# Kernel tuning notes

Measured on AMD Instinct MI355X. Metric: run time of the kernel, lower is better.

Reference implementation:

```python
import jax, jax.numpy as jnp
import numpy as np
from jax.scipy.special import logsumexp

L, B, C, H = 1024, 256, 96, 768
STD = (1.0 / C) ** 0.5


def setup_inputs() -> dict:
    key = jax.random.key(0)
    ks = jax.random.split(key, 8)
    emit = jax.random.normal(ks[0], (L, B, C), dtype=jnp.float32)
    hidden = jax.random.normal(ks[1], (B, H), dtype=jnp.float32)
    target = jax.random.randint(ks[2], (L, B), 0, C)
    # variable sentence lengths in [L//2, L]; mask[0] is always True
    lens = jax.random.randint(ks[3], (B,), L // 2, L + 1)
    mask = jnp.arange(L)[:, None] < lens[None, :]
    Wt = jax.random.normal(ks[4], (C * C, H), dtype=jnp.float32) * STD
    bt = jnp.zeros((C * C,), dtype=jnp.float32)
    Ws = jax.random.normal(ks[5], (C, H), dtype=jnp.float32) * STD
    bs = jnp.zeros((C,), dtype=jnp.float32)
    We = jax.random.normal(ks[6], (C, H), dtype=jnp.float32) * STD
    be = jnp.zeros((C,), dtype=jnp.float32)
    return {"emit": emit, "hidden": hidden, "target": target, "mask": mask,
            "Wt": Wt, "bt": bt, "Ws": Ws, "bs": bs, "We": We, "be": be}


def _crf_loss(emit, hidden, target, mask, Wt, bt, Ws, bs, We, be):
    l, b, c = emit.shape
    trans = (hidden @ Wt.T + bt).reshape(b, c, c)          # [B, prev, next]
    t_start = hidden @ Ws.T + bs                           # [B, C]
    t_end = hidden @ We.T + be                             # [B, C]

    # ---- log partition (forward algorithm), sequential scan over time ----
    def step(log_alpha, xs):
        emit_i, mask_i = xs                                # [B,C], [B]
        # scores[b,p,n] = log_alpha[b,p] + trans[b,p,n] + emit_i[b,n]
        new = logsumexp(log_alpha[:, :, None] + trans + emit_i[:, None, :], axis=1)
        log_alpha = jnp.where(mask_i[:, None], new, log_alpha)
        return log_alpha, None

    log_alpha0 = emit[0] + t_start
    log_alpha, _ = jax.lax.scan(step, log_alpha0, (emit[1:], mask[1:]))
    log_z = logsumexp(log_alpha + t_end, axis=1).sum()

    # ---- gold path score ----
    bidx = jnp.arange(b)
    tr_sc = trans[bidx[None, :], target[:-1], target[1:]]          # [L-1, B]
    emit_sc = jnp.take_along_axis(emit, target[:, :, None], axis=2)[:, :, 0]  # [L, B]
    scores = emit_sc.at[1:].add(tr_sc)
    score = jnp.sum(scores * mask.astype(emit.dtype))
    ends = mask.sum(axis=0) - 1                                    # [B]
    last_tag = target[ends, bidx]
    score = score + t_start[bidx, target[0]].sum() + t_end[bidx, last_tag].sum()

    return (log_z - score) / b


def reference(emit, hidden, target, mask, Wt, bt, Ws, bs, We, be):
    return _crf_loss(emit, hidden, target, mask, Wt, bt, Ws, bs, We, be)
```

## Files before the change

### kernel.cpp

```cpp
#include <hip/hip_runtime.h>
#include <hip/hip_bf16.h>
#include <stdint.h>

#define LL 1024
#define BB 256
#define CC 96
#define HH 768
#define NW 9216
#define NTOT 9408
#define SEGS 8
#define SEGLEN 128
#define CHPB 15

typedef __attribute__((ext_vector_type(4))) float floatx4;
typedef __attribute__((ext_vector_type(2))) float floatx2;
typedef __attribute__((ext_vector_type(8))) short short8;

#define KAPPA 0x1p-16f
#define NEG_LOG_KAPPA 11.090354888959125f

__device__ __forceinline__ unsigned short f2bf(float f) {
  uint32_t u = __float_as_uint(f);
  return (unsigned short)((u + 0x7FFFu + ((u >> 16) & 1u)) >> 16);
}

#define GA_LD 40

__global__ __launch_bounds__(256) void gemm_mfma(
    const float* __restrict__ hidden, const float* __restrict__ Wt,
    const float* __restrict__ Ws, const float* __restrict__ We,
    const float* __restrict__ bt, const float* __restrict__ bs,
    const float* __restrict__ be, float* __restrict__ trans,
    float* __restrict__ tstart, float* __restrict__ tend) {
  __shared__ __align__(16) unsigned short As[128 * GA_LD];
  __shared__ __align__(16) unsigned short Bs[128 * GA_LD];
  const int t = threadIdx.x;
  const int lane = t & 63, wid = t >> 6;
  const int wm = wid >> 1, wn = wid & 1;
  const int l15 = lane & 15, qd = lane >> 4;
  const int m0 = blockIdx.y * 128, n0 = blockIdx.x * 128;
  const int srow = t >> 1, shalf = t & 1;

  floatx4 acc[4][4];
#pragma unroll
  for (int i = 0; i < 4; ++i)
#pragma unroll
    for (int j = 0; j < 4; ++j) acc[i][j] = (floatx4){0.f, 0.f, 0.f, 0.f};

  const int r = n0 + srow;
  const float* bsrc = (r < NW)        ? Wt + (size_t)r * HH
                      : (r < NW + CC) ? Ws + (size_t)(r - NW) * HH
                      : (r < NTOT)    ? We + (size_t)(r - NW - CC) * HH
                                      : nullptr;
  const float* asrc = hidden + (size_t)(m0 + srow) * HH;
  const int sidx = srow * GA_LD + shalf * 16;

  for (int k0 = 0; k0 < HH; k0 += 32) {
    __syncthreads();
    {
      const float4* s4 = (const float4*)(asrc + k0 + shalf * 16);
      uint32_t w[8];
#pragma unroll
      for (int u = 0; u < 4; ++u) {
        float4 v = s4[u];
        w[2 * u] = (uint32_t)f2bf(v.x) | ((uint32_t)f2bf(v.y) << 16);
        w[2 * u + 1] = (uint32_t)f2bf(v.z) | ((uint32_t)f2bf(v.w) << 16);
      }
      *(uint4*)&As[sidx] = make_uint4(w[0], w[1], w[2], w[3]);
      *(uint4*)&As[sidx + 8] = make_uint4(w[4], w[5], w[6], w[7]);
    }
    {
      uint32_t w[8];
      if (bsrc) {
        const float4* s4 = (const float4*)(bsrc + k0 + shalf * 16);
#pragma unroll
        for (int u = 0; u < 4; ++u) {
          float4 v = s4[u];
          w[2 * u] = (uint32_t)f2bf(v.x) | ((uint32_t)f2bf(v.y) << 16);
          w[2 * u + 1] = (uint32_t)f2bf(v.z) | ((uint32_t)f2bf(v.w) << 16);
        }
      } else {
#pragma unroll
        for (int u = 0; u < 8; ++u) w[u] = 0u;
      }
      *(uint4*)&Bs[sidx] = make_uint4(w[0], w[1], w[2], w[3]);
      *(uint4*)&Bs[sidx + 8] = make_uint4(w[4], w[5], w[6], w[7]);
    }
    __syncthreads();
    short8 af[4], bf[4];
#pragma unroll
    for (int i = 0; i < 4; ++i)
      af[i] = *(const short8*)&As[(64 * wm + 16 * i + l15) * GA_LD + qd * 8];
#pragma unroll
    for (int j = 0; j < 4; ++j)
      bf[j] = *(const short8*)&Bs[(64 * wn + 16 * j + l15) * GA_LD + qd * 8];
#pragma unroll
    for (int i = 0; i < 4; ++i)
#pragma unroll
      for (int j = 0; j < 4; ++j)
        acc[i][j] = __builtin_amdgcn_mfma_f32_16x16x32_bf16(af[i], bf[j],
                                                            acc[i][j], 0, 0, 0);
  }

#pragma unroll
  for (int j = 0; j < 4; ++j) {
    int n = n0 + 64 * wn + 16 * j + l15;
    if (n >= NTOT) continue;
    float bv;
    float* dst;
    int ldo;
    if (n < NW) {
      bv = bt[n]; dst = trans + n; ldo = NW;
    } else if (n < NW + CC) {
      bv = bs[n - NW]; dst = tstart + (n - NW); ldo = CC;
    } else {
      bv = be[n - NW - CC]; dst = tend + (n - NW - CC); ldo = CC;
    }
#pragma unroll
    for (int i = 0; i < 4; ++i)
#pragma unroll
      for (int rr = 0; rr < 4; ++rr) {
        int m = m0 + 64 * wm + 16 * i + 4 * qd + rr;
        dst[(size_t)m * ldo] = acc[i][j][rr] + bv;
      }
  }
}

__device__ __forceinline__ float wredf(float v) {
#pragma unroll
  for (int m = 32; m >= 1; m >>= 1) v += __shfl_xor(v, m);
  return v;
}
__device__ __forceinline__ int wredi(int v) {
#pragma unroll
  for (int m = 32; m >= 1; m >>= 1) v += __shfl_xor(v, m);
  return v;
}
__device__ __forceinline__ float bcast0(float x) {
  return __uint_as_float(__builtin_amdgcn_readfirstlane(__float_as_uint(x)));
}
__device__ __forceinline__ int get_len(const void* mask, int b, int l) {
  int cnt = 0;
  unsigned w0 = *(const unsigned*)mask;
  if (w0 == 1u) {
    const int* m32 = (const int*)mask;
    for (int i = l; i < LL; i += 64) cnt += (m32[i * BB + b] != 0);
  } else if (w0 == 0x01010101u) {
    const unsigned char* m8 = (const unsigned char*)mask;
    for (int i = l; i < LL; i += 64) cnt += (m8[i * BB + b] != 0);
  } else {
    const float* mf = (const float*)mask;
    for (int i = l; i < LL; i += 64) cnt += (mf[i * BB + b] != 0.f);
  }
  return wredi(cnt);
}

__global__ __launch_bounds__(64, 1) void crf_chain(
    const float* __restrict__ emit, const void* __restrict__ mask,
    const float* __restrict__ trans, const float* __restrict__ tstart,
    float* __restrict__ xvec, float* __restrict__ lsc) {
  const int blk = blockIdx.x;
  const int b = blk >> 3;
  const int k = blk & 7;
  const bool isfw = (k < 4);
  int segA, segB;
  bool hasB;
  if (isfw) {
    segA = k; segB = k + 4; hasB = true;
  } else if (k < 7) {
    segA = k - 3; segB = k + 1; hasB = true;
  } else {
    segA = 4; segB = 0; hasB = false;
  }
  const int l = threadIdx.x;
  const int pr = l >> 1, s = l & 1;

  __shared__ __align__(16) float ebA[2][8][CC];
  __shared__ __align__(16) float uAv[CC];
  __shared__ __align__(16) float ebB[2][8][CC];
  __shared__ __align__(16) float uBv[CC];

  const int len = get_len(mask, b, l);
  const int loA = segA * SEGLEN + 1;
  const int hiA = min((segA + 1) * SEGLEN, len - 1);
  const int loB = segB * SEGLEN + 1;
  const int hiB = hasB ? min((segB + 1) * SEGLEN, len - 1) : -1;
  const int cidA = b * CHPB + (isfw ? segA : 7 + segA);
  const int cidB = b * CHPB + (isfw ? segB : 7 + segB);
  const bool actB = hasB && (hiB >= loB);
  const int nA = hiA - loA + 1;
  const int nB = actB ? (hiB - loB + 1) : 0;

  if (hasB && !actB) {
    float* xo = xvec + (size_t)cidB * CC;
    xo[l] = 1.f;
    if (l < 32) xo[l + 64] = 1.f;
    if (l == 0) lsc[cidB] = 0.f;
  }
  if (hiA < loA) {
    float* xo = xvec + (size_t)cidA * CC;
    xo[l] = 1.f;
    if (l < 32) xo[l + 64] = 1.f;
    if (l == 0) lsc[cidA] = 0.f;
    return;
  }

  const float* tb = trans + (size_t)b * (CC * CC);
  floatx2 T2[3][24];
  if (isfw) {
#pragma unroll
    for (int j = 0; j < 24; ++j) {
      const float* r0 = tb + (48 * s + 2 * j) * CC + 3 * pr;
      const float* r1 = r0 + CC;
#pragma unroll
      for (int o = 0; o < 3; ++o)
        T2[o][j] = (floatx2){__expf(r0[o]), __expf(r1[o])};
    }
  } else {
#pragma unroll
    for (int o = 0; o < 3; ++o) {
      const float* row = tb + (3 * pr + o) * CC + 48 * s;
#pragma unroll
      for (int j = 0; j < 24; ++j)
        T2[o][j] = (floatx2){__expf(row[2 * j]), __expf(row[2 * j + 1])};
    }
  }

  const float4* e4 = (const float4*)emit;
  const int eoff = 3 * pr + 2 * s;
  float LA = 0.f, pvA = 1.f, LB = 0.f, pvB = 1.f;

#define CLOB asm volatile("" ::: "memory")

  auto STAGE = [&](float (*eb)[8][CC], int baserow, int slot) {
#pragma unroll
    for (int uu = 0; uu < 3; ++uu) {
      int v = l + 64 * uu;
      int rw = v / 24, c4 = v - 24 * rw;
      float4 vv = e4[((baserow + rw) * BB + b) * 24 + c4];
      floatx4 o = {__expf(vv.x) * KAPPA, __expf(vv.y) * KAPPA,
                   __expf(vv.z) * KAPPA, __expf(vv.w) * KAPPA};
      *(floatx4*)&eb[slot][rw][c4 * 4] = o;
    }
  };

  auto DOT = [&](const float* ub, float& a0, float& a1, float& a2) {
    const floatx4* up = (const floatx4*)&ub[48 * s];
    floatx2 A0 = {0.f, 0.f}, B0 = {0.f, 0.f};
    floatx2 A1 = {0.f, 0.f}, B1 = {0.f, 0.f};
    floatx2 A2 = {0.f, 0.f}, B2 = {0.f, 0.f};
#pragma unroll
    for (int j4 = 0; j4 < 12; ++j4) {
      floatx4 U = up[j4];
      floatx2 lo2 = {U.x, U.y}, hi2 = {U.z, U.w};
      A0 += lo2 * T2[0][2 * j4]; B0 += hi2 * T2[0][2 * j4 + 1];
      A1 += lo2 * T2[1][2 * j4]; B1 += hi2 * T2[1][2 * j4 + 1];
      A2 += lo2 * T2[2][2 * j4]; B2 += hi2 * T2[2][2 * j4 + 1];
    }
    floatx2 S0 = A0 + B0, S1 = A1 + B1, S2 = A2 + B2;
    a0 = S0.x + S0.y; a1 = S1.x + S1.y; a2 = S2.x + S2.y;
    a0 += __shfl_xor(a0, 1);
    a1 += __shfl_xor(a1, 1);
    a2 += __shfl_xor(a2, 1);
  };

  auto STEPF = [&](int i, int jjv, float& pvv, float& Lv,
                   float (*eb)[8][CC], float* ub) {
    float invP = 1.f;
    if ((jjv & 3) == 0) { invP = 1.0f / pvv; Lv += __logf(pvv); }
    float a0, a1, a2;
    DOT(ub, a0, a1, a2);
    floatx2 E = *(const floatx2*)&eb[(i >> 3) & 1][i & 7][eoff];
    float o0 = a0 * E.x * invP;
    if (((jjv + 1) & 3) == 0) pvv = bcast0(o0);
    if (s == 0) {
      floatx2 wv = {o0, a1 * E.y * invP};
      *(floatx2*)&ub[3 * pr] = wv;
    } else {
      ub[3 * pr + 2] = a2 * E.x * invP;
    }
  };

  auto STEPB = [&](int i, int lo, int jjv, float& pvv, float& Lv,
                   float (*eb)[8][CC], float* ub) {
    float invP = 1.f;
    if ((jjv & 3) == 0) { invP = 1.0f / pvv; Lv += __logf(pvv); }
    float a0, a1, a2;
    DOT(ub, a0, a1, a2);
    floatx2 E = (i > lo)
        ? *(const floatx2*)&eb[((i - 1) >> 3) & 1][(i - 1) & 7][eoff]
        : (floatx2){1.f, 1.f};
    float o0 = a0 * E.x * invP;
    if (((jjv + 1) & 3) == 0) pvv = bcast0(o0);
    if (s == 0) {
      floatx2 wv = {o0, a1 * E.y * invP};
      *(floatx2*)&ub[3 * pr] = wv;
    } else {
      ub[3 * pr + 2] = a2 * E.x * invP;
    }
  };

  if (isfw) {
    const int bA0 = loA & ~7;
    STAGE(ebA, bA0, (bA0 >> 3) & 1);
    if (actB) {
      const int bB0 = loB & ~7;
      STAGE(ebB, bB0, (bB0 >> 3) & 1);
    }
    if (segA == 0) {
      float a00 = emit[(size_t)b * CC] + tstart[b * CC];
      LA = a00;
      float v = emit[(size_t)b * CC + l] + tstart[b * CC + l];
      uAv[l] = __expf(v - a00);
      if (l < 32) {
        int c2 = l + 64;
        float v2 = emit[(size_t)b * CC + c2] + tstart[b * CC + c2];
        uAv[c2] = __expf(v2 - a00);
      }
    } else {
      uAv[l] = 1.f;
      if (l < 32) uAv[l + 64] = 1.f;
    }
    if (actB) {
      uBv[l] = 1.f;
      if (l < 32) uBv[l + 64] = 1.f;
    }
    CLOB;
    int jj = 1;
    int iA = loA, iB = loB;
    const int nmin = actB ? min(nA, nB) : 0;
    for (; jj <= nmin; ++jj, ++iA, ++iB) {
      bool st = false;
      if ((iA & 7) == 0) { STAGE(ebA, iA, (iA >> 3) & 1); st = true; }
      if ((iB & 7) == 0) { STAGE(ebB, iB, (iB >> 3) & 1); st = true; }
      if (st) CLOB;
      STEPF(iA, jj, pvA, LA, ebA, uAv);
      STEPF(iB, jj, pvB, LB, ebB, uBv);
      CLOB;
    }
    int jjA = jj;
    for (; iA <= hiA; ++iA, ++jjA) {
      if ((iA & 7) == 0) { STAGE(ebA, iA, (iA >> 3) & 1); CLOB; }
      STEPF(iA, jjA, pvA, LA, ebA, uAv);
      CLOB;
    }
    int jjB = jj;
    for (; actB && iB <= hiB; ++iB, ++jjB) {
      if ((iB & 7) == 0) { STAGE(ebB, iB, (iB >> 3) & 1); CLOB; }
      STEPF(iB, jjB, pvB, LB, ebB, uBv);
      CLOB;
    }
  } else {
    const int cA0 = hiA & ~7;
    STAGE(ebA, cA0, (cA0 >> 3) & 1);
    if (actB) {
      const int cB0 = hiB & ~7;
      STAGE(ebB, cB0, (cB0 >> 3) & 1);
    }
    CLOB;
    uAv[l] = ebA[(hiA >> 3) & 1][hiA & 7][l];
    if (l < 32) uAv[l + 64] = ebA[(hiA >> 3) & 1][hiA & 7][l + 64];
    if (actB) {
      uBv[l] = ebB[(hiB >> 3) & 1][hiB & 7][l];
      if (l < 32) uBv[l + 64] = ebB[(hiB >> 3) & 1][hiB & 7][l + 64];
    }
    CLOB;
    int jj = 1;
    int iA = hiA, iB = hiB;
    const int nmin = actB ? min(nA, nB) : 0;
    for (; jj <= nmin; ++jj, --iA, --iB) {
      bool st = false;
      if ((iA & 7) == 0 && iA > loA) {
        STAGE(ebA, iA - 8, ((iA >> 3) & 1) ^ 1); st = true;
      }
      if ((iB & 7) == 0 && iB > loB) {
        STAGE(ebB, iB - 8, ((iB >> 3) & 1) ^ 1); st = true;
      }
      if (st) CLOB;
      STEPB(iA, loA, jj, pvA, LA, ebA, uAv);
      STEPB(iB, loB, jj, pvB, LB, ebB, uBv);
      CLOB;
    }
    int jjA = jj;
    for (; iA >= loA; --iA, ++jjA) {
      if ((iA & 7) == 0 && iA > loA) {
        STAGE(ebA, iA - 8, ((iA >> 3) & 1) ^ 1); CLOB;
      }
      STEPB(iA, loA, jjA, pvA, LA, ebA, uAv);
      CLOB;
    }
    int jjB = jj;
    for (; actB && iB >= loB; --iB, ++jjB) {
      if ((iB & 7) == 0 && iB > loB) {
        STAGE(ebB, iB - 8, ((iB >> 3) & 1) ^ 1); CLOB;
      }
      STEPB(iB, loB, jjB, pvB, LB, ebB, uBv);
      CLOB;
    }
  }

  CLOB;
  {
    float* xo = xvec + (size_t)cidA * CC;
    xo[l] = uAv[l];
    if (l < 32) xo[l + 64] = uAv[l + 64];
    if (l == 0) lsc[cidA] = LA + (float)nA * NEG_LOG_KAPPA;
  }
  if (actB) {
    float* xo = xvec + (size_t)cidB * CC;
    xo[l] = uBv[l];
    if (l < 32) xo[l + 64] = uBv[l + 64];
    if (l == 0) lsc[cidB] = LB + (float)nB * NEG_LOG_KAPPA;
  }
}

__global__ __launch_bounds__(64) void crf_compose(
    const float* __restrict__ emit, const int* __restrict__ target,
    const void* __restrict__ mask, const float* __restrict__ trans,
    const float* __restrict__ tstart, const float* __restrict__ tend,
    const float* __restrict__ xvec, const float* __restrict__ lsc,
    float* __restrict__ out) {
  const int b = blockIdx.x;
  const int l = threadIdx.x;
  const int len = get_len(mask, b, l);

  float Lam = lsc[b * CHPB + 0];
  const float* xcur = xvec + (size_t)(b * CHPB + 0) * CC;
  for (int s2 = 1; s2 < SEGS; ++s2) {
    if (s2 * SEGLEN + 1 > len - 1) break;
    const float* bh = xvec + (size_t)(b * CHPB + (SEGS - 1) + s2) * CC;
    const float* ah = xvec + (size_t)(b * CHPB + s2) * CC;
    float pn = bh[l] * xcur[l];
    float pd = bh[l];
    if (l < 32) {
      pn += bh[l + 64] * xcur[l + 64];
      pd += bh[l + 64];
    }
    float num = wredf(pn), den = wredf(pd);
    Lam += __logf(num / den) + lsc[b * CHPB + s2];
    xcur = ah;
  }
  float zp = xcur[l] * __expf(tend[b * CC + l]);
  if (l < 32) zp += xcur[l + 64] * __expf(tend[b * CC + l + 64]);
  float logz = Lam + __logf(wredf(zp));

  const float* tb = trans + (size_t)b * (CC * CC);
  float sc = 0.f;
  for (int i = l; i < len; i += 64) {
    int tg = target[i * BB + b];
    sc += emit[((size_t)i * BB + b) * CC + tg];
    if (i >= 1) sc += tb[target[(i - 1) * BB + b] * CC + tg];
  }
  float score = wredf(sc);
  if (l == 0) {
    score += tstart[b * CC + target[b]] +
             tend[b * CC + target[(len - 1) * BB + b]];
    atomicAdd(out, (logz - score) * (1.0f / 256.0f));
  }
}

extern "C" void kernel_launch(void* const* d_in, const int* in_sizes, int n_in,
                              void* d_out, int out_size, void* d_ws, size_t ws_size,
                              hipStream_t stream) {
  const float* emit = (const float*)d_in[0];
  const float* hidden = (const float*)d_in[1];
  const int* target = (const int*)d_in[2];
  const void* mask = d_in[3];
  const float* Wt = (const float*)d_in[4];
  const float* bt = (const float*)d_in[5];
  const float* Ws = (const float*)d_in[6];
  const float* bs = (const float*)d_in[7];
  const float* We = (const float*)d_in[8];
  const float* be = (const float*)d_in[9];

  float* trans_ws = (float*)d_ws;
  float* ts_ws = trans_ws + (size_t)BB * CC * CC;
  float* te_ws = ts_ws + (size_t)BB * CC;
  float* xvec = te_ws + (size_t)BB * CC;
  float* lsc = xvec + (size_t)BB * CHPB * CC;

  hipMemsetAsync(d_out, 0, sizeof(float), stream);

  gemm_mfma<<<dim3((NTOT + 127) / 128, 2), 256, 0, stream>>>(
      hidden, Wt, Ws, We, bt, bs, be, trans_ws, ts_ws, te_ws);

  crf_chain<<<BB * 8, 64, 0, stream>>>(emit, mask, trans_ws, ts_ws, xvec, lsc);

  crf_compose<<<BB, 64, 0, stream>>>(emit, target, mask, trans_ws, ts_ws, te_ws,
                                     xvec, lsc, (float*)d_out);
}
```

Measured before the change: 442.3 us.

## Split chain dot across four lanes with DPP reduction and fused dual-chain step

```diff
diff --git a/kernel.cpp b/kernel.cpp
--- a/kernel.cpp
+++ b/kernel.cpp
@@ -139,6 +139,11 @@
 __device__ __forceinline__ float bcast0(float x) {
   return __uint_as_float(__builtin_amdgcn_readfirstlane(__float_as_uint(x)));
 }
+__device__ __forceinline__ float qsum4(float x) {
+  x += __int_as_float(__builtin_amdgcn_mov_dpp(__float_as_int(x), 0xB1, 0xF, 0xF, false));
+  x += __int_as_float(__builtin_amdgcn_mov_dpp(__float_as_int(x), 0x4E, 0xF, 0xF, false));
+  return x;
+}
 __device__ __forceinline__ int get_len(const void* mask, int b, int l) {
   int cnt = 0;
   unsigned w0 = *(const unsigned*)mask;
@@ -163,33 +168,28 @@
   const int b = blk >> 3;
   const int k = blk & 7;
   const bool isfw = (k < 4);
-  int segA, segB;
+  int segA, segB = 0;
   bool hasB;
-  if (isfw) {
-    segA = k; segB = k + 4; hasB = true;
-  } else if (k < 7) {
-    segA = k - 3; segB = k + 1; hasB = true;
-  } else {
-    segA = 4; segB = 0; hasB = false;
-  }
+  if (isfw) { segA = 2 * k; segB = 2 * k + 1; hasB = true; }
+  else if (k < 7) { segA = 2 * (k - 4) + 1; segB = segA + 1; hasB = true; }
+  else { segA = 7; hasB = false; }
   const int l = threadIdx.x;
-  const int pr = l >> 1, s = l & 1;
+  const int g = l >> 2, q = l & 3;
 
   __shared__ __align__(16) float ebA[2][8][CC];
-  __shared__ __align__(16) float uAv[CC];
+  __shared__ __align__(16) float uA[CC];
   __shared__ __align__(16) float ebB[2][8][CC];
-  __shared__ __align__(16) float uBv[CC];
+  __shared__ __align__(16) float uB[CC];
 
   const int len = get_len(mask, b, l);
   const int loA = segA * SEGLEN + 1;
   const int hiA = min((segA + 1) * SEGLEN, len - 1);
-  const int loB = segB * SEGLEN + 1;
+  const int loB = hasB ? segB * SEGLEN + 1 : 0;
   const int hiB = hasB ? min((segB + 1) * SEGLEN, len - 1) : -1;
+  const bool actA = hiA >= loA;
+  const bool actB = hasB && (hiB >= loB);
   const int cidA = b * CHPB + (isfw ? segA : 7 + segA);
-  const int cidB = b * CHPB + (isfw ? segB : 7 + segB);
-  const bool actB = hasB && (hiB >= loB);
-  const int nA = hiA - loA + 1;
-  const int nB = actB ? (hiB - loB + 1) : 0;
+  const int cidB = hasB ? (b * CHPB + (isfw ? segB : 7 + segB)) : 0;
 
   if (hasB && !actB) {
     float* xo = xvec + (size_t)cidB * CC;
@@ -197,204 +197,231 @@
     if (l < 32) xo[l + 64] = 1.f;
     if (l == 0) lsc[cidB] = 0.f;
   }
-  if (hiA < loA) {
+  if (!actA) {
     float* xo = xvec + (size_t)cidA * CC;
     xo[l] = 1.f;
     if (l < 32) xo[l + 64] = 1.f;
     if (l == 0) lsc[cidA] = 0.f;
     return;
   }
+  const int nA = hiA - loA + 1;
+  const int nB = actB ? (hiB - loB + 1) : 0;
 
   const float* tb = trans + (size_t)b * (CC * CC);
-  floatx2 T2[3][24];
+  floatx2 T2[6][12];
   if (isfw) {
 #pragma unroll
-    for (int j = 0; j < 24; ++j) {
-      const float* r0 = tb + (48 * s + 2 * j) * CC + 3 * pr;
-      const float* r1 = r0 + CC;
-#pragma unroll
-      for (int o = 0; o < 3; ++o)
-        T2[o][j] = (floatx2){__expf(r0[o]), __expf(r1[o])};
-    }
+    for (int t = 0; t < 6; ++t)
+#pragma unroll
+      for (int m = 0; m < 12; ++m) {
+        const float* p0 = tb + (24 * q + 2 * m) * CC + 6 * g + t;
+        T2[t][m] = (floatx2){__expf(p0[0]), __expf(p0[CC])};
+      }
   } else {
 #pragma unroll
-    for (int o = 0; o < 3; ++o) {
-      const float* row = tb + (3 * pr + o) * CC + 48 * s;
-#pragma unroll
-      for (int j = 0; j < 24; ++j)
-        T2[o][j] = (floatx2){__expf(row[2 * j]), __expf(row[2 * j + 1])};
+    for (int t = 0; t < 6; ++t) {
+      const float* row = tb + (6 * g + t) * CC + 24 * q;
+#pragma unroll
+      for (int m = 0; m < 12; ++m)
+        T2[t][m] = (floatx2){__expf(row[2 * m]), __expf(row[2 * m + 1])};
     }
   }
 
   const float4* e4 = (const float4*)emit;
-  const int eoff = 3 * pr + 2 * s;
+  const int eidx = 6 * g + 2 * (q < 3 ? q : 2);
   float LA = 0.f, pvA = 1.f, LB = 0.f, pvB = 1.f;
 
 #define CLOB asm volatile("" ::: "memory")
 
-  auto STAGE = [&](float (*eb)[8][CC], int baserow, int slot) {
-#pragma unroll
-    for (int uu = 0; uu < 3; ++uu) {
-      int v = l + 64 * uu;
-      int rw = v / 24, c4 = v - 24 * rw;
-      float4 vv = e4[((baserow + rw) * BB + b) * 24 + c4];
-      floatx4 o = {__expf(vv.x) * KAPPA, __expf(vv.y) * KAPPA,
-                   __expf(vv.z) * KAPPA, __expf(vv.w) * KAPPA};
-      *(floatx4*)&eb[slot][rw][c4 * 4] = o;
-    }
-  };
-
-  auto DOT = [&](const float* ub, float& a0, float& a1, float& a2) {
-    const floatx4* up = (const floatx4*)&ub[48 * s];
-    floatx2 A0 = {0.f, 0.f}, B0 = {0.f, 0.f};
-    floatx2 A1 = {0.f, 0.f}, B1 = {0.f, 0.f};
-    floatx2 A2 = {0.f, 0.f}, B2 = {0.f, 0.f};
-#pragma unroll
-    for (int j4 = 0; j4 < 12; ++j4) {
-      floatx4 U = up[j4];
-      floatx2 lo2 = {U.x, U.y}, hi2 = {U.z, U.w};
-      A0 += lo2 * T2[0][2 * j4]; B0 += hi2 * T2[0][2 * j4 + 1];
-      A1 += lo2 * T2[1][2 * j4]; B1 += hi2 * T2[1][2 * j4 + 1];
-      A2 += lo2 * T2[2][2 * j4]; B2 += hi2 * T2[2][2 * j4 + 1];
-    }
-    floatx2 S0 = A0 + B0, S1 = A1 + B1, S2 = A2 + B2;
-    a0 = S0.x + S0.y; a1 = S1.x + S1.y; a2 = S2.x + S2.y;
-    a0 += __shfl_xor(a0, 1);
-    a1 += __shfl_xor(a1, 1);
-    a2 += __shfl_xor(a2, 1);
-  };
-
-  auto STEPF = [&](int i, int jjv, float& pvv, float& Lv,
-                   float (*eb)[8][CC], float* ub) {
-    float invP = 1.f;
-    if ((jjv & 3) == 0) { invP = 1.0f / pvv; Lv += __logf(pvv); }
-    float a0, a1, a2;
-    DOT(ub, a0, a1, a2);
-    floatx2 E = *(const floatx2*)&eb[(i >> 3) & 1][i & 7][eoff];
-    float o0 = a0 * E.x * invP;
-    if (((jjv + 1) & 3) == 0) pvv = bcast0(o0);
-    if (s == 0) {
-      floatx2 wv = {o0, a1 * E.y * invP};
-      *(floatx2*)&ub[3 * pr] = wv;
-    } else {
-      ub[3 * pr + 2] = a2 * E.x * invP;
-    }
-  };
-
-  auto STEPB = [&](int i, int lo, int jjv, float& pvv, float& Lv,
-                   float (*eb)[8][CC], float* ub) {
-    float invP = 1.f;
-    if ((jjv & 3) == 0) { invP = 1.0f / pvv; Lv += __logf(pvv); }
-    float a0, a1, a2;
-    DOT(ub, a0, a1, a2);
-    floatx2 E = (i > lo)
-        ? *(const floatx2*)&eb[((i - 1) >> 3) & 1][(i - 1) & 7][eoff]
-        : (floatx2){1.f, 1.f};
-    float o0 = a0 * E.x * invP;
-    if (((jjv + 1) & 3) == 0) pvv = bcast0(o0);
-    if (s == 0) {
-      floatx2 wv = {o0, a1 * E.y * invP};
-      *(floatx2*)&ub[3 * pr] = wv;
-    } else {
-      ub[3 * pr + 2] = a2 * E.x * invP;
-    }
-  };
+#define STAGE_CHUNK(EB, baserow, slot)                                    \
+  {                                                                       \
+    _Pragma("unroll") for (int uu = 0; uu < 3; ++uu) {                    \
+      int v = l + 64 * uu;                                                \
+      int rw = v / 24, c4 = v - 24 * rw;                                  \
+      float4 vv = e4[(((baserow) + rw) * BB + b) * 24 + c4];              \
+      floatx4 o = {__expf(vv.x) * KAPPA, __expf(vv.y) * KAPPA,            \
+                   __expf(vv.z) * KAPPA, __expf(vv.w) * KAPPA};           \
+      *(floatx4*)&EB[slot][rw][c4 * 4] = o;                               \
+    }                                                                     \
+  }
+
+#define INNER_DOT6(UU, aV)                                                \
+  float aV[6];                                                            \
+  {                                                                       \
+    const floatx4* up_ = (const floatx4*)&UU[24 * q];                     \
+    floatx4 R_[6];                                                        \
+    _Pragma("unroll") for (int nn = 0; nn < 6; ++nn) R_[nn] = up_[nn];    \
+    floatx2 P_[6], Q_[6];                                                 \
+    _Pragma("unroll") for (int t = 0; t < 6; ++t) {                       \
+      P_[t] = (floatx2){0.f, 0.f}; Q_[t] = (floatx2){0.f, 0.f};           \
+    }                                                                     \
+    _Pragma("unroll") for (int nn = 0; nn < 6; ++nn) {                    \
+      floatx2 lo_ = {R_[nn].x, R_[nn].y}, hi_ = {R_[nn].z, R_[nn].w};     \
+      _Pragma("unroll") for (int t = 0; t < 6; ++t) {                     \
+        P_[t] += lo_ * T2[t][2 * nn]; Q_[t] += hi_ * T2[t][2 * nn + 1];   \
+      }                                                                   \
+    }                                                                     \
+    _Pragma("unroll") for (int t = 0; t < 6; ++t) {                       \
+      floatx2 S_ = P_[t] + Q_[t];                                         \
+      aV[t] = qsum4(S_.x + S_.y);                                         \
+    }                                                                     \
+  }
+
+#define DUAL_DOT6(aAv, aBv)                                               \
+  float aAv[6], aBv[6];                                                   \
+  {                                                                       \
+    const floatx4* upA_ = (const floatx4*)&uA[24 * q];                    \
+    const floatx4* upB_ = (const floatx4*)&uB[24 * q];                    \
+    floatx4 RA_[6], RB_[6];                                               \
+    _Pragma("unroll") for (int nn = 0; nn < 6; ++nn) {                    \
+      RA_[nn] = upA_[nn]; RB_[nn] = upB_[nn];                             \
+    }                                                                     \
+    floatx2 PA_[6], QA_[6], PB_[6], QB_[6];                               \
+    _Pragma("unroll") for (int t = 0; t < 6; ++t) {                       \
+      PA_[t] = (floatx2){0.f, 0.f}; QA_[t] = (floatx2){0.f, 0.f};         \
+      PB_[t] = (floatx2){0.f, 0.f}; QB_[t] = (floatx2){0.f, 0.f};         \
+    }                                                                     \
+    _Pragma("unroll") for (int nn = 0; nn < 6; ++nn) {                    \
+      floatx2 la_ = {RA_[nn].x, RA_[nn].y}, ha_ = {RA_[nn].z, RA_[nn].w}; \
+      floatx2 lb_ = {RB_[nn].x, RB_[nn].y}, hb_ = {RB_[nn].z, RB_[nn].w}; \
+      _Pragma("unroll") for (int t = 0; t < 6; ++t) {                     \
+        PA_[t] += la_ * T2[t][2 * nn]; QA_[t] += ha_ * T2[t][2 * nn + 1]; \
+        PB_[t] += lb_ * T2[t][2 * nn]; QB_[t] += hb_ * T2[t][2 * nn + 1]; \
+      }                                                                   \
+    }                                                                     \
+    _Pragma("unroll") for (int t = 0; t < 6; ++t) {                       \
+      floatx2 S_ = PA_[t] + QA_[t];                                       \
+      aAv[t] = qsum4(S_.x + S_.y);                                        \
+      S_ = PB_[t] + QB_[t];                                               \
+      aBv[t] = qsum4(S_.x + S_.y);                                        \
+    }                                                                     \
+  }
+
+#define WRITE_U(UU, aV, Ex_, Ey_, invP_)                                  \
+  {                                                                       \
+    float wx = (q == 0) ? aV[0] : ((q == 1) ? aV[2] : aV[4]);             \
+    float wy = (q == 0) ? aV[1] : ((q == 1) ? aV[3] : aV[5]);             \
+    if (q < 3) {                                                          \
+      floatx2 wv = {wx * (Ex_) * (invP_), wy * (Ey_) * (invP_)};          \
+      *(floatx2*)&UU[6 * g + 2 * q] = wv;                                 \
+    }                                                                     \
+  }
 
   if (isfw) {
     const int bA0 = loA & ~7;
-    STAGE(ebA, bA0, (bA0 >> 3) & 1);
+    STAGE_CHUNK(ebA, bA0, (bA0 >> 3) & 1);
     if (actB) {
       const int bB0 = loB & ~7;
-      STAGE(ebB, bB0, (bB0 >> 3) & 1);
+      STAGE_CHUNK(ebB, bB0, (bB0 >> 3) & 1);
     }
     if (segA == 0) {
       float a00 = emit[(size_t)b * CC] + tstart[b * CC];
       LA = a00;
       float v = emit[(size_t)b * CC + l] + tstart[b * CC + l];
-      uAv[l] = __expf(v - a00);
+      uA[l] = __expf(v - a00);
       if (l < 32) {
         int c2 = l + 64;
         float v2 = emit[(size_t)b * CC + c2] + tstart[b * CC + c2];
-        uAv[c2] = __expf(v2 - a00);
+        uA[c2] = __expf(v2 - a00);
       }
     } else {
-      uAv[l] = 1.f;
-      if (l < 32) uAv[l + 64] = 1.f;
+      uA[l] = 1.f;
+      if (l < 32) uA[l + 64] = 1.f;
     }
     if (actB) {
-      uBv[l] = 1.f;
-      if (l < 32) uBv[l + 64] = 1.f;
+      uB[l] = 1.f;
+      if (l < 32) uB[l + 64] = 1.f;
     }
     CLOB;
-    int jj = 1;
-    int iA = loA, iB = loB;
-    const int nmin = actB ? min(nA, nB) : 0;
-    for (; jj <= nmin; ++jj, ++iA, ++iB) {
+    int jj = 1, iA = loA, iB = loB;
+    for (; jj <= nB; ++jj, ++iA, ++iB) {
       bool st = false;
-      if ((iA & 7) == 0) { STAGE(ebA, iA, (iA >> 3) & 1); st = true; }
-      if ((iB & 7) == 0) { STAGE(ebB, iB, (iB >> 3) & 1); st = true; }
+      if ((iA & 7) == 0) { STAGE_CHUNK(ebA, iA, (iA >> 3) & 1); st = true; }
+      if ((iB & 7) == 0) { STAGE_CHUNK(ebB, iB, (iB >> 3) & 1); st = true; }
       if (st) CLOB;
-      STEPF(iA, jj, pvA, LA, ebA, uAv);
-      STEPF(iB, jj, pvB, LB, ebB, uBv);
+      float invPA = 1.f, invPB = 1.f;
+      if ((jj & 3) == 0) {
+        invPA = 1.0f / pvA; LA += __logf(pvA);
+        invPB = 1.0f / pvB; LB += __logf(pvB);
+      }
+      DUAL_DOT6(aA, aB);
+      floatx2 EA = *(const floatx2*)&ebA[(iA >> 3) & 1][iA & 7][eidx];
+      floatx2 EBv = *(const floatx2*)&ebB[(iB >> 3) & 1][iB & 7][eidx];
+      float o0A = aA[0] * EA.x * invPA;
+      float o0B = aB[0] * EBv.x * invPB;
+      if (((jj + 1) & 3) == 0) { pvA = bcast0(o0A); pvB = bcast0(o0B); }
+      WRITE_U(uA, aA, EA.x, EA.y, invPA);
+      WRITE_U(uB, aB, EBv.x, EBv.y, invPB);
       CLOB;
     }
-    int jjA = jj;
-    for (; iA <= hiA; ++iA, ++jjA) {
-      if ((iA & 7) == 0) { STAGE(ebA, iA, (iA >> 3) & 1); CLOB; }
-      STEPF(iA, jjA, pvA, LA, ebA, uAv);
-      CLOB;
-    }
-    int jjB = jj;
-    for (; actB && iB <= hiB; ++iB, ++jjB) {
-      if ((iB & 7) == 0) { STAGE(ebB, iB, (iB >> 3) & 1); CLOB; }
-      STEPF(iB, jjB, pvB, LB, ebB, uBv);
+    for (; iA <= hiA; ++iA, ++jj) {
+      if ((iA & 7) == 0) { STAGE_CHUNK(ebA, iA, (iA >> 3) & 1); CLOB; }
+      float invP = 1.f;
+      if ((jj & 3) == 0) { invP = 1.0f / pvA; LA += __logf(pvA); }
+      INNER_DOT6(uA, aS);
+      floatx2 E = *(const floatx2*)&ebA[(iA >> 3) & 1][iA & 7][eidx];
+      float o0 = aS[0] * E.x * invP;
+      if (((jj + 1) & 3) == 0) pvA = bcast0(o0);
+      WRITE_U(uA, aS, E.x, E.y, invP);
       CLOB;
     }
   } else {
     const int cA0 = hiA & ~7;
-    STAGE(ebA, cA0, (cA0 >> 3) & 1);
+    STAGE_CHUNK(ebA, cA0, (cA0 >> 3) & 1);
     if (actB) {
       const int cB0 = hiB & ~7;
-      STAGE(ebB, cB0, (cB0 >> 3) & 1);
+      STAGE_CHUNK(ebB, cB0, (cB0 >> 3) & 1);
     }
     CLOB;
-    uAv[l] = ebA[(hiA >> 3) & 1][hiA & 7][l];
-    if (l < 32) uAv[l + 64] = ebA[(hiA >> 3) & 1][hiA & 7][l + 64];
+    uA[l] = ebA[(hiA >> 3) & 1][hiA & 7][l];
+    if (l < 32) uA[l + 64] = ebA[(hiA >> 3) & 1][hiA & 7][l + 64];
     if (actB) {
-      uBv[l] = ebB[(hiB >> 3) & 1][hiB & 7][l];
-      if (l < 32) uBv[l + 64] = ebB[(hiB >> 3) & 1][hiB & 7][l + 64];
+      uB[l] = ebB[(hiB >> 3) & 1][hiB & 7][l];
+      if (l < 32) uB[l + 64] = ebB[(hiB >> 3) & 1][hiB & 7][l + 64];
     }
     CLOB;
-    int jj = 1;
-    int iA = hiA, iB = hiB;
-    const int nmin = actB ? min(nA, nB) : 0;
-    for (; jj <= nmin; ++jj, --iA, --iB) {
+    int jj = 1, iA = hiA, iB = hiB;
+    for (; jj <= nB; ++jj, --iA, --iB) {
       bool st = false;
       if ((iA & 7) == 0 && iA > loA) {
-        STAGE(ebA, iA - 8, ((iA >> 3) & 1) ^ 1); st = true;
+        STAGE_CHUNK(ebA, iA - 8, ((iA >> 3) & 1) ^ 1); st = true;
       }
       if ((iB & 7) == 0 && iB > loB) {
-        STAGE(ebB, iB - 8, ((iB >> 3) & 1) ^ 1); st = true;
+        STAGE_CHUNK(ebB, iB - 8, ((iB >> 3) & 1) ^ 1); st = true;
       }
       if (st) CLOB;
-      STEPB(iA, loA, jj, pvA, LA, ebA, uAv);
-      STEPB(iB, loB, jj, pvB, LB, ebB, uBv);
+      float invPA = 1.f, invPB = 1.f;
+      if ((jj & 3) == 0) {
+        invPA = 1.0f / pvA; LA += __logf(pvA);
+        invPB = 1.0f / pvB; LB += __logf(pvB);
+      }
+      DUAL_DOT6(aA, aB);
+      floatx2 EA = (iA > loA)
+          ? *(const floatx2*)&ebA[((iA - 1) >> 3) & 1][(iA - 1) & 7][eidx]
+          : (floatx2){1.f, 1.f};
+      floatx2 EBv = (iB > loB)
+          ? *(const floatx2*)&ebB[((iB - 1) >> 3) & 1][(iB - 1) & 7][eidx]
+          : (floatx2){1.f, 1.f};
+      float o0A = aA[0] * EA.x * invPA;
+      float o0B = aB[0] * EBv.x * invPB;
+      if (((jj + 1) & 3) == 0) { pvA = bcast0(o0A); pvB = bcast0(o0B); }
+      WRITE_U(uA, aA, EA.x, EA.y, invPA);
+      WRITE_U(uB, aB, EBv.x, EBv.y, invPB);
       CLOB;
     }
-    int jjA = jj;
-    for (; iA >= loA; --iA, ++jjA) {
+    for (; iA >= loA; --iA, ++jj) {
       if ((iA & 7) == 0 && iA > loA) {
-        STAGE(ebA, iA - 8, ((iA >> 3) & 1) ^ 1); CLOB;
-      }
-      STEPB(iA, loA, jjA, pvA, LA, ebA, uAv);
-      CLOB;
-    }
-    int jjB = jj;
-    for (; actB && iB >= loB; --iB, ++jjB) {
-      if ((iB & 7) == 0 && iB > loB) {
-        STAGE(ebB, iB - 8, ((iB >> 3) & 1) ^ 1); CLOB;
-      }
-      STEPB(iB, loB, jjB, pvB, LB, ebB, uBv);
+        STAGE_CHUNK(ebA, iA - 8, ((iA >> 3) & 1) ^ 1); CLOB;
+      }
+      float invP = 1.f;
+      if ((jj & 3) == 0) { invP = 1.0f / pvA; LA += __logf(pvA); }
+      INNER_DOT6(uA, aS);
+      floatx2 E = (iA > loA)
+          ? *(const floatx2*)&ebA[((iA - 1) >> 3) & 1][(iA - 1) & 7][eidx]
+          : (floatx2){1.f, 1.f};
+      float o0 = aS[0] * E.x * invP;
+      if (((jj + 1) & 3) == 0) pvA = bcast0(o0);
+      WRITE_U(uA, aS, E.x, E.y, invP);
       CLOB;
     }
   }
@@ -402,14 +429,14 @@
   CLOB;
   {
     float* xo = xvec + (size_t)cidA * CC;
-    xo[l] = uAv[l];
-    if (l < 32) xo[l + 64] = uAv[l + 64];
+    xo[l] = uA[l];
+    if (l < 32) xo[l + 64] = uA[l + 64];
     if (l == 0) lsc[cidA] = LA + (float)nA * NEG_LOG_KAPPA;
   }
   if (actB) {
     float* xo = xvec + (size_t)cidB * CC;
-    xo[l] = uBv[l];
-    if (l < 32) xo[l + 64] = uBv[l + 64];
+    xo[l] = uB[l];
+    if (l < 32) xo[l + 64] = uB[l + 64];
     if (l == 0) lsc[cidB] = LB + (float)nB * NEG_LOG_KAPPA;
   }
 }
```

Measured after the change: 474.0 us. +7.2%, slower.
